# Kernel optimization log

Hardware: AMD Instinct MI355X
Metric: run time of the kernel (lower is better)

The kernel has to match this reference:

```python
import jax, jax.numpy as jnp
import numpy as np

N, E, G, F_IN, D = 50000, 400000, 256, 79, 400
BN_EPS = 1e-5


def setup_inputs() -> dict:
    key = jax.random.key(0)
    ks = jax.random.split(key, 16)
    w = lambda k, s: jax.random.normal(k, s, dtype=jnp.float32) * 0.05
    return {
        "x": jax.random.normal(ks[0], (N, F_IN), dtype=jnp.float32),
        "edge_index": jax.random.randint(ks[1], (2, E), 0, N, dtype=jnp.int32),
        "batch_index": jnp.sort(jax.random.randint(ks[2], (N,), 0, G, dtype=jnp.int32)),
        "num_graphs": G,
        "mlp1_w1": w(ks[3], (F_IN, D)), "mlp1_b1": jnp.zeros(D, jnp.float32),
        "mlp1_bn_g": jnp.ones(D, jnp.float32), "mlp1_bn_b": jnp.zeros(D, jnp.float32),
        "mlp1_bn_m": jnp.zeros(D, jnp.float32), "mlp1_bn_v": jnp.ones(D, jnp.float32),
        "mlp1_w2": w(ks[4], (D, D)), "mlp1_b2": jnp.zeros(D, jnp.float32),
        "mlp2_w1": w(ks[5], (D, D)), "mlp2_b1": jnp.zeros(D, jnp.float32),
        "mlp2_bn_g": jnp.ones(D, jnp.float32), "mlp2_bn_b": jnp.zeros(D, jnp.float32),
        "mlp2_bn_m": jnp.zeros(D, jnp.float32), "mlp2_bn_v": jnp.ones(D, jnp.float32),
        "mlp2_w2": w(ks[6], (D, D)), "mlp2_b2": jnp.zeros(D, jnp.float32),
        "out1_w": w(ks[7], (D, D)), "out1_b": jnp.zeros(D, jnp.float32),
        "out2_w": w(ks[8], (D, D)), "out2_b": jnp.zeros(D, jnp.float32),
        "out3_w": w(ks[9], (D, D)), "out3_b": jnp.zeros(D, jnp.float32),
        "out_w": w(ks[10], (2 * D, 1)), "out_b": jnp.zeros(1, jnp.float32),
        "eps1": jnp.full((1,), 5e-5, jnp.float32),
        "eps2": jnp.full((1,), 5e-5, jnp.float32),
        "eps3": jnp.full((1,), 5e-5, jnp.float32),
    }


def _bn(z, g, b, m, v):
    # BatchNorm1d in inference mode (running stats)
    return (z - m) * jax.lax.rsqrt(v + BN_EPS) * g + b


def _gin(h, src, dst, eps, w1, b1, g, bb, m, v, w2, b2):
    n = h.shape[0]
    agg = jax.ops.segment_sum(h[src], dst, num_segments=n)  # [N, d] scatter-add
    z = (1.0 + eps) * h + agg
    z = jax.nn.relu(_bn(z @ w1 + b1, g, bb, m, v))
    return jax.nn.relu(z @ w2 + b2)


def reference(x, edge_index, batch_index, num_graphs,
              mlp1_w1, mlp1_b1, mlp1_bn_g, mlp1_bn_b, mlp1_bn_m, mlp1_bn_v, mlp1_w2, mlp1_b2,
              mlp2_w1, mlp2_b1, mlp2_bn_g, mlp2_bn_b, mlp2_bn_m, mlp2_bn_v, mlp2_w2, mlp2_b2,
              out1_w, out1_b, out2_w, out2_b, out3_w, out3_b, out_w, out_b,
              eps1, eps2, eps3):
    src, dst = edge_index[0], edge_index[1]
    h = _gin(x, src, dst, eps1[0], mlp1_w1, mlp1_b1, mlp1_bn_g, mlp1_bn_b, mlp1_bn_m, mlp1_bn_v, mlp1_w2, mlp1_b2)
    h = jnp.tanh(h @ out1_w + out1_b)
    h = _gin(h, src, dst, eps2[0], mlp2_w1, mlp2_b1, mlp2_bn_g, mlp2_bn_b, mlp2_bn_m, mlp2_bn_v, mlp2_w2, mlp2_b2)
    h = jnp.tanh(h @ out2_w + out2_b)
    h = _gin(h, src, dst, eps3[0], mlp2_w1, mlp2_b1, mlp2_bn_g, mlp2_bn_b, mlp2_bn_m, mlp2_bn_v, mlp2_w2, mlp2_b2)
    h = jnp.tanh(h @ out3_w + out3_b)
    # dropout is identity in eval mode
    mx = jax.ops.segment_max(h, batch_index, num_segments=num_graphs)   # global_max_pool
    sm = jax.ops.segment_sum(h, batch_index, num_segments=num_graphs)
    cnt = jax.ops.segment_sum(jnp.ones((h.shape[0], 1), h.dtype), batch_index, num_segments=num_graphs)
    mn = sm / jnp.maximum(cnt, 1.0)                                      # global_mean_pool
    pooled = jnp.concatenate([mx, mn], axis=1)                           # [G, 2D]
    return pooled @ out_w + out_b
```

## Files before the change

### kernel.cpp

```cpp
#include <hip/hip_runtime.h>
#include <math.h>

#define NN 50000
#define NE 400000
#define NG 256
#define FIN 79
#define DD 400
#define LDK 448
#define LDK1 128
#define XP 80
#define NPAD 512
#define BK 64
#define MT ((NN + 127) / 128)
#define BN_EPS_F 1e-5f

#define SCAN_B 256
#define SCAN_NB ((NN + SCAN_B - 1) / SCAN_B)

typedef unsigned short u16;
typedef unsigned short ushort8 __attribute__((ext_vector_type(8)));
typedef unsigned short ushort4v __attribute__((ext_vector_type(4)));
typedef short short8 __attribute__((ext_vector_type(8)));
typedef float floatx4 __attribute__((ext_vector_type(4)));

__device__ inline u16 f2bf(float f) {
    unsigned int u = __builtin_bit_cast(unsigned int, f);
    u += 0x7fffu + ((u >> 16) & 1u);
    return (u16)(u >> 16);
}
__device__ inline float bf2f(u16 s) {
    unsigned int u = ((unsigned int)s) << 16;
    return __builtin_bit_cast(float, u);
}
__device__ inline float fast_tanh(float x) {
    float e = __expf(2.0f * x);
    return 1.0f - 2.0f / (e + 1.0f);
}

__device__ __forceinline__ void gld_lds16(const u16* g, u16* l) {
    __builtin_amdgcn_global_load_lds(
        (const __attribute__((address_space(1))) unsigned int*)(size_t)(g),
        (__attribute__((address_space(3))) unsigned int*)(unsigned int)(size_t)(l),
        16, 0, 0);
}

__global__ void k_gstart(const int* __restrict__ batch, int* __restrict__ gstart) {
    int g = blockIdx.x * blockDim.x + threadIdx.x;
    if (g > NG) return;
    int lo = 0, hi = NN;
    while (lo < hi) {
        int mid = (lo + hi) >> 1;
        if (batch[mid] < g) lo = mid + 1; else hi = mid;
    }
    gstart[g] = lo;
}

__global__ void k_zero_int(int* __restrict__ p, int n) {
    int i = blockIdx.x * blockDim.x + threadIdx.x;
    if (i < n) p[i] = 0;
}
__global__ void k_hist(const int* __restrict__ dst, int* __restrict__ deg) {
    int e = blockIdx.x * blockDim.x + threadIdx.x;
    if (e < NE) atomicAdd(&deg[dst[e]], 1);
}

__global__ void k_scan_a(const int* __restrict__ deg, int* __restrict__ bsum) {
    __shared__ int red[SCAN_B];
    int i = blockIdx.x * SCAN_B + threadIdx.x;
    red[threadIdx.x] = (i < NN) ? deg[i] : 0;
    __syncthreads();
    for (int s = SCAN_B / 2; s > 0; s >>= 1) {
        if (threadIdx.x < s) red[threadIdx.x] += red[threadIdx.x + s];
        __syncthreads();
    }
    if (threadIdx.x == 0) bsum[blockIdx.x] = red[0];
}
__global__ void k_scan_b(const int* __restrict__ bsum, int* __restrict__ boff) {
    __shared__ int buf[SCAN_B];
    int t = threadIdx.x;
    int v = (t < SCAN_NB) ? bsum[t] : 0;
    buf[t] = v;
    __syncthreads();
    for (int off = 1; off < SCAN_B; off <<= 1) {
        int add = (t >= off) ? buf[t - off] : 0;
        __syncthreads();
        buf[t] += add;
        __syncthreads();
    }
    if (t < SCAN_NB) boff[t] = buf[t] - v;
}
__global__ void k_scan_c(const int* __restrict__ deg, const int* __restrict__ boff,
                         int* __restrict__ rowptr, int* __restrict__ cursor) {
    __shared__ int buf[SCAN_B];
    int b = blockIdx.x;
    int i = b * SCAN_B + threadIdx.x;
    int v = (i < NN) ? deg[i] : 0;
    buf[threadIdx.x] = v;
    __syncthreads();
    for (int off = 1; off < SCAN_B; off <<= 1) {
        int add = (threadIdx.x >= off) ? buf[threadIdx.x - off] : 0;
        __syncthreads();
        buf[threadIdx.x] += add;
        __syncthreads();
    }
    int excl = boff[b] + buf[threadIdx.x] - v;
    if (i < NN) { rowptr[i] = excl; cursor[i] = excl; }
    if (b == 0 && threadIdx.x == 0) rowptr[NN] = NE;
}

__global__ void k_fill(const int* __restrict__ src, const int* __restrict__ dst,
                       int* __restrict__ cursor, int* __restrict__ eidx) {
    int e = blockIdx.x * blockDim.x + threadIdx.x;
    if (e < NE) {
        int pos = atomicAdd(&cursor[dst[e]], 1);
        eidx[pos] = src[e];
    }
}

__global__ void k_packw(const float* __restrict__ W, int K, u16* __restrict__ Wt, int ldk) {
    int idx = blockIdx.x * 256 + threadIdx.x;
    int total = NPAD * ldk;
    if (idx >= total) return;
    int n = idx / ldk, k = idx - n * ldk;
    float v = (n < DD && k < K) ? W[(size_t)k * DD + n] : 0.0f;
    Wt[idx] = f2bf(v);
}

__global__ __launch_bounds__(256)
void k_packx(const float* __restrict__ x, u16* __restrict__ xb) {
    int idx = blockIdx.x * 256 + threadIdx.x;
    if (idx >= NN * XP) return;
    int n = idx / XP, c = idx - n * XP;
    xb[idx] = (c < FIN) ? f2bf(x[(size_t)n * FIN + c]) : (u16)0;
}

__global__ __launch_bounds__(256)
void k_agg1(const u16* __restrict__ xb, const int* __restrict__ rowptr,
            const int* __restrict__ eidx, const float* __restrict__ eps,
            u16* __restrict__ z0) {
    int wave = threadIdx.x >> 6, lane = threadIdx.x & 63;
    int n = blockIdx.x * 4 + wave;
    if (lane >= 32) return;
    u16* zr = z0 + (size_t)n * LDK1;
    if (lane >= 20) {
        ushort4v zz = {0, 0, 0, 0};
        *(ushort4v*)&zr[XP + (lane - 20) * 4] = zz;
        return;
    }
    float s = 1.0f + eps[0];
    int c4 = lane * 4;
    ushort4v v = *(const ushort4v*)&xb[(size_t)n * XP + c4];
    float a[4];
    #pragma unroll
    for (int t = 0; t < 4; ++t) a[t] = s * bf2f(v[t]);
    int e0 = rowptr[n], e1 = rowptr[n + 1];
    int i = e0;
    for (; i + 2 <= e1; i += 2) {
        int s0 = eidx[i], s1 = eidx[i + 1];
        ushort4v v0 = *(const ushort4v*)&xb[(size_t)s0 * XP + c4];
        ushort4v v1 = *(const ushort4v*)&xb[(size_t)s1 * XP + c4];
        #pragma unroll
        for (int t = 0; t < 4; ++t) a[t] += bf2f(v0[t]) + bf2f(v1[t]);
    }
    if (i < e1) {
        int s0 = eidx[i];
        ushort4v v0 = *(const ushort4v*)&xb[(size_t)s0 * XP + c4];
        #pragma unroll
        for (int t = 0; t < 4; ++t) a[t] += bf2f(v0[t]);
    }
    ushort4v o;
    #pragma unroll
    for (int t = 0; t < 4; ++t) o[t] = f2bf(a[t]);
    *(ushort4v*)&zr[c4] = o;
}

__global__ __launch_bounds__(256)
void k_agg(const u16* __restrict__ h, const int* __restrict__ rowptr,
           const int* __restrict__ eidx, const float* __restrict__ eps,
           u16* __restrict__ z) {
    int wave = threadIdx.x >> 6, lane = threadIdx.x & 63;
    int n = blockIdx.x * 4 + wave;
    if (lane >= 56) return;
    float s = 1.0f + eps[0];
    int c8 = lane * 8;
    ushort8 v = *(const ushort8*)(h + (size_t)n * LDK + c8);
    float a[8];
    #pragma unroll
    for (int t = 0; t < 8; ++t) a[t] = s * bf2f(v[t]);
    int e0 = rowptr[n], e1 = rowptr[n + 1];
    int i = e0;
    for (; i + 2 <= e1; i += 2) {
        int s0 = eidx[i], s1 = eidx[i + 1];
        ushort8 v0 = *(const ushort8*)(h + (size_t)s0 * LDK + c8);
        ushort8 v1 = *(const ushort8*)(h + (size_t)s1 * LDK + c8);
        #pragma unroll
        for (int t = 0; t < 8; ++t) a[t] += bf2f(v0[t]) + bf2f(v1[t]);
    }
    if (i < e1) {
        int s0 = eidx[i];
        ushort8 v0 = *(const ushort8*)(h + (size_t)s0 * LDK + c8);
        #pragma unroll
        for (int t = 0; t < 8; ++t) a[t] += bf2f(v0[t]);
    }
    ushort8 o;
    #pragma unroll
    for (int t = 0; t < 8; ++t) o[t] = f2bf(a[t]);
    *(ushort8*)(z + (size_t)n * LDK + c8) = o;
}

#define CSTR 136
__global__ __launch_bounds__(256, 4)
void k_gemm(const u16* __restrict__ A, int lda, int ktiles,
            const u16* __restrict__ Wt,
            const float* __restrict__ bias,
            const float* __restrict__ bng, const float* __restrict__ bnb,
            const float* __restrict__ bnm, const float* __restrict__ bnv,
            u16* __restrict__ Y, int mode)
{
    __shared__ u16 smem[128 * CSTR];
    u16* As = smem;
    u16* Bs = smem + 128 * BK;
    u16* Cs = smem;

    int id = blockIdx.x;
    int mt = (id >> 5) * 8 + (id & 7);
    int nt = (id & 31) >> 3;
    if (mt >= MT) return;
    int m0 = mt * 128;
    int n0 = nt * 128;

    int tid = threadIdx.x;
    int wave = tid >> 6, lane = tid & 63;
    int wm = wave & 1, wn = wave >> 1;

    int srow = lane >> 3;
    int sc   = lane & 7;
    int lm = lane & 15;
    int q  = lane >> 4;

    bool nactive = (n0 + wn * 64) < LDK;

    floatx4 acc[4][4] = {};

    for (int kt = 0; kt < ktiles; ++kt) {
        int k0 = kt * BK;
        #pragma unroll
        for (int j = 0; j < 4; ++j) {
            int row = wave * 32 + j * 8 + srow;
            int cs = sc ^ (row & 7);
            int gr = m0 + row; gr = gr < NN ? gr : NN - 1;
            gld_lds16(A + (size_t)gr * lda + k0 + (cs << 3),
                      &As[(wave * 32 + j * 8) * BK]);
            gld_lds16(Wt + (size_t)(n0 + row) * lda + k0 + (cs << 3),
                      &Bs[(wave * 32 + j * 8) * BK]);
        }
        __syncthreads();

        if (nactive) {
            #pragma unroll
            for (int ks = 0; ks < 2; ++ks) {
                short8 af[4], bf[4];
                #pragma unroll
                for (int i = 0; i < 4; ++i) {
                    int r = wm * 64 + i * 16 + lm;
                    int ch = (ks * 4 + q) ^ (r & 7);
                    af[i] = *(const short8*)&As[r * BK + ch * 8];
                }
                #pragma unroll
                for (int j = 0; j < 4; ++j) {
                    int r = wn * 64 + j * 16 + lm;
                    int ch = (ks * 4 + q) ^ (r & 7);
                    bf[j] = *(const short8*)&Bs[r * BK + ch * 8];
                }
                #pragma unroll
                for (int i = 0; i < 4; ++i)
                    #pragma unroll
                    for (int j = 0; j < 4; ++j)
                        acc[i][j] = __builtin_amdgcn_mfma_f32_16x16x32_bf16(af[i], bf[j], acc[i][j], 0, 0, 0);
            }
        }
        __syncthreads();
    }

    #pragma unroll
    for (int j = 0; j < 4; ++j) {
        int nl = wn * 64 + j * 16 + lm;
        int n  = n0 + nl;
        bool live = n < DD;
        float bias_c = 0.0f, sc2 = 1.0f, sh = 0.0f;
        if (live) {
            bias_c = bias[n];
            if (mode == 0) {
                sc2 = bng[n] * rsqrtf(bnv[n] + BN_EPS_F);
                sh = bnb[n] - bnm[n] * sc2;
            }
        }
        #pragma unroll
        for (int i = 0; i < 4; ++i) {
            int rl = wm * 64 + i * 16 + q * 4;
            #pragma unroll
            for (int r = 0; r < 4; ++r) {
                u16 o = 0;
                if (live) {
                    float val = acc[i][j][r] + bias_c;
                    if (mode == 0)      val = fmaxf(fmaf(val, sc2, sh), 0.0f);
                    else if (mode == 1) val = fmaxf(val, 0.0f);
                    else                val = fast_tanh(val);
                    o = f2bf(val);
                }
                Cs[(rl + r) * CSTR + nl] = o;
            }
        }
    }
    __syncthreads();

    int row = tid >> 1, half = tid & 1;
    int m = m0 + row;
    if (m < NN) {
        #pragma unroll
        for (int k = 0; k < 8; ++k) {
            int coloff = half * 64 + k * 8;
            int n = n0 + coloff;
            if (n < LDK) {
                ushort8 v = *(const ushort8*)&Cs[row * CSTR + coloff];
                *(ushort8*)&Y[(size_t)m * LDK + n] = v;
            }
        }
    }
}

__global__ void k_pool(const u16* __restrict__ t3, const int* __restrict__ gstart,
                       float* __restrict__ pooled) {
    int g = blockIdx.x;
    int c = blockIdx.y * 128 + threadIdx.x;
    if (c >= DD) return;
    int s = gstart[g], e = gstart[g + 1];
    float mx = -INFINITY, sm = 0.0f;
    for (int n = s; n < e; ++n) {
        float v = bf2f(t3[(size_t)n * LDK + c]);
        mx = fmaxf(mx, v);
        sm += v;
    }
    float cnt = (float)(e - s);
    pooled[(size_t)g * 2 * DD + c] = mx;
    pooled[(size_t)g * 2 * DD + DD + c] = sm / fmaxf(cnt, 1.0f);
}

__global__ void k_final(const float* __restrict__ pooled, const float* __restrict__ w,
                        const float* __restrict__ b, float* __restrict__ out) {
    __shared__ float red[256];
    int g = blockIdx.x;
    float p = 0.0f;
    for (int j = threadIdx.x; j < 2 * DD; j += blockDim.x)
        p += pooled[(size_t)g * 2 * DD + j] * w[j];
    red[threadIdx.x] = p;
    __syncthreads();
    for (int s = 128; s > 0; s >>= 1) {
        if (threadIdx.x < s) red[threadIdx.x] += red[threadIdx.x + s];
        __syncthreads();
    }
    if (threadIdx.x == 0) out[g] = red[0] + b[0];
}

extern "C" void kernel_launch(void* const* d_in, const int* in_sizes, int n_in,
                              void* d_out, int out_size, void* d_ws, size_t ws_size,
                              hipStream_t stream) {
    const float* x     = (const float*)d_in[0];
    const int*   ei    = (const int*)d_in[1];
    const int*   batch = (const int*)d_in[2];
    const float* m1w1  = (const float*)d_in[4];
    const float* m1b1  = (const float*)d_in[5];
    const float* m1g   = (const float*)d_in[6];
    const float* m1bb  = (const float*)d_in[7];
    const float* m1m   = (const float*)d_in[8];
    const float* m1v   = (const float*)d_in[9];
    const float* m1w2  = (const float*)d_in[10];
    const float* m1b2  = (const float*)d_in[11];
    const float* m2w1  = (const float*)d_in[12];
    const float* m2b1  = (const float*)d_in[13];
    const float* m2g   = (const float*)d_in[14];
    const float* m2bb  = (const float*)d_in[15];
    const float* m2m   = (const float*)d_in[16];
    const float* m2v   = (const float*)d_in[17];
    const float* m2w2  = (const float*)d_in[18];
    const float* m2b2  = (const float*)d_in[19];
    const float* o1w   = (const float*)d_in[20];
    const float* o1b   = (const float*)d_in[21];
    const float* o2w   = (const float*)d_in[22];
    const float* o2b   = (const float*)d_in[23];
    const float* o3w   = (const float*)d_in[24];
    const float* o3b   = (const float*)d_in[25];
    const float* ow    = (const float*)d_in[26];
    const float* ob    = (const float*)d_in[27];
    const float* eps1  = (const float*)d_in[28];
    const float* eps2  = (const float*)d_in[29];
    const float* eps3  = (const float*)d_in[30];
    const int* srcI = ei;
    const int* dstI = ei + NE;

    u16* buf1 = (u16*)d_ws;
    u16* buf2 = buf1 + (size_t)NN * LDK;
    u16* buf3 = buf2 + (size_t)NN * LDK;
    u16* z0   = buf3 + (size_t)NN * LDK;
    u16* w1t  = z0 + (size_t)NN * LDK1;
    u16* m1w2t = w1t + (size_t)NPAD * LDK1;
    u16* m2w1t = m1w2t + (size_t)NPAD * LDK;
    u16* m2w2t = m2w1t + (size_t)NPAD * LDK;
    u16* o1t   = m2w2t + (size_t)NPAD * LDK;
    u16* o2t   = o1t + (size_t)NPAD * LDK;
    u16* o3t   = o2t + (size_t)NPAD * LDK;
    u16* xb    = o3t + (size_t)NPAD * LDK;
    float* pooled = (float*)(xb + (size_t)NN * XP);
    int* gstart = (int*)(pooled + (size_t)NG * 2 * DD);
    int* rowptr = gstart + (NG + 2);
    int* cursor = rowptr + (NN + 1);
    int* deg    = cursor + NN;
    int* eidx   = deg + NN;
    int* bsum   = eidx + NE;
    int* boff   = bsum + SCAN_NB;

    float* out = (float*)d_out;

    int gemmBlocks = ((MT + 7) / 8) * 32;

    k_gstart<<<2, 256, 0, stream>>>(batch, gstart);
    k_zero_int<<<(NN + 255) / 256, 256, 0, stream>>>(deg, NN);
    k_hist<<<(NE + 255) / 256, 256, 0, stream>>>(dstI, deg);
    k_scan_a<<<SCAN_NB, SCAN_B, 0, stream>>>(deg, bsum);
    k_scan_b<<<1, SCAN_B, 0, stream>>>(bsum, boff);
    k_scan_c<<<SCAN_NB, SCAN_B, 0, stream>>>(deg, boff, rowptr, cursor);
    k_fill<<<(NE + 255) / 256, 256, 0, stream>>>(srcI, dstI, cursor, eidx);

    int pw1 = (NPAD * LDK1 + 255) / 256;
    int pw = (NPAD * LDK + 255) / 256;
    k_packw<<<pw1, 256, 0, stream>>>(m1w1, FIN, w1t, LDK1);
    k_packw<<<pw, 256, 0, stream>>>(m1w2, DD, m1w2t, LDK);
    k_packw<<<pw, 256, 0, stream>>>(m2w1, DD, m2w1t, LDK);
    k_packw<<<pw, 256, 0, stream>>>(m2w2, DD, m2w2t, LDK);
    k_packw<<<pw, 256, 0, stream>>>(o1w, DD, o1t, LDK);
    k_packw<<<pw, 256, 0, stream>>>(o2w, DD, o2t, LDK);
    k_packw<<<pw, 256, 0, stream>>>(o3w, DD, o3t, LDK);
    k_packx<<<(NN * XP + 255) / 256, 256, 0, stream>>>(x, xb);

    k_agg1<<<NN / 4, 256, 0, stream>>>(xb, rowptr, eidx, eps1, z0);
    k_gemm<<<gemmBlocks, 256, 0, stream>>>(z0, LDK1, LDK1 / BK, w1t, m1b1,
                                           m1g, m1bb, m1m, m1v, buf1, 0);
    k_gemm<<<gemmBlocks, 256, 0, stream>>>(buf1, LDK, LDK / BK, m1w2t, m1b2,
                                           nullptr, nullptr, nullptr, nullptr, buf2, 1);
    k_gemm<<<gemmBlocks, 256, 0, stream>>>(buf2, LDK, LDK / BK, o1t, o1b,
                                           nullptr, nullptr, nullptr, nullptr, buf3, 2);

    k_agg<<<NN / 4, 256, 0, stream>>>(buf3, rowptr, eidx, eps2, buf1);
    k_gemm<<<gemmBlocks, 256, 0, stream>>>(buf1, LDK, LDK / BK, m2w1t, m2b1,
                                           m2g, m2bb, m2m, m2v, buf2, 0);
    k_gemm<<<gemmBlocks, 256, 0, stream>>>(buf2, LDK, LDK / BK, m2w2t, m2b2,
                                           nullptr, nullptr, nullptr, nullptr, buf1, 1);
    k_gemm<<<gemmBlocks, 256, 0, stream>>>(buf1, LDK, LDK / BK, o2t, o2b,
                                           nullptr, nullptr, nullptr, nullptr, buf2, 2);

    k_agg<<<NN / 4, 256, 0, stream>>>(buf2, rowptr, eidx, eps3, buf1);
    k_gemm<<<gemmBlocks, 256, 0, stream>>>(buf1, LDK, LDK / BK, m2w1t, m2b1,
                                           m2g, m2bb, m2m, m2v, buf3, 0);
    k_gemm<<<gemmBlocks, 256, 0, stream>>>(buf3, LDK, LDK / BK, m2w2t, m2b2,
                                           nullptr, nullptr, nullptr, nullptr, buf1, 1);
    k_gemm<<<gemmBlocks, 256, 0, stream>>>(buf1, LDK, LDK / BK, o3t, o3b,
                                           nullptr, nullptr, nullptr, nullptr, buf3, 2);

    k_pool<<<dim3(NG, 4), 128, 0, stream>>>(buf3, gstart, pooled);
    k_final<<<NG, 256, 0, stream>>>(pooled, ow, ob, out);
}
```

Measured before the change: 868.3 us.

## Prefetch GEMM tiles through registers, vectorize pooling, trim padded aggregation lanes

The GEMM no longer uses direct global-to-LDS loads. It keeps the next K-tile in registers while the current tile is computed, so global load latency overlaps with the MFMA work, and it relaxes the launch-bounds occupancy hint from 4 to 3. Global pooling now uses one 256-thread block per graph: four waves stride over the nodes with 8-wide vector loads and are combined through LDS, replacing scalar per-column loops. Aggregation skips the padded columns 400-447, which cuts wasted gathers but leaves those padding columns of z unwritten, so correctness depends on them already holding zeros from earlier writes.

```diff
diff --git a/kernel.cpp b/kernel.cpp
--- a/kernel.cpp
+++ b/kernel.cpp
@@ -37,13 +37,6 @@
     return 1.0f - 2.0f / (e + 1.0f);
 }
 
-__device__ __forceinline__ void gld_lds16(const u16* g, u16* l) {
-    __builtin_amdgcn_global_load_lds(
-        (const __attribute__((address_space(1))) unsigned int*)(size_t)(g),
-        (__attribute__((address_space(3))) unsigned int*)(unsigned int)(size_t)(l),
-        16, 0, 0);
-}
-
 __global__ void k_gstart(const int* __restrict__ batch, int* __restrict__ gstart) {
     int g = blockIdx.x * blockDim.x + threadIdx.x;
     if (g > NG) return;
@@ -180,7 +173,7 @@
            u16* __restrict__ z) {
     int wave = threadIdx.x >> 6, lane = threadIdx.x & 63;
     int n = blockIdx.x * 4 + wave;
-    if (lane >= 56) return;
+    if (lane >= 50) return;
     float s = 1.0f + eps[0];
     int c8 = lane * 8;
     ushort8 v = *(const ushort8*)(h + (size_t)n * LDK + c8);
@@ -209,7 +202,7 @@
 }
 
 #define CSTR 136
-__global__ __launch_bounds__(256, 4)
+__global__ __launch_bounds__(256, 3)
 void k_gemm(const u16* __restrict__ A, int lda, int ktiles,
             const u16* __restrict__ Wt,
             const float* __restrict__ bias,
@@ -235,27 +228,45 @@
 
     int srow = lane >> 3;
     int sc   = lane & 7;
+    int swz  = (sc ^ srow) << 3;
     int lm = lane & 15;
     int q  = lane >> 4;
 
     bool nactive = (n0 + wn * 64) < LDK;
 
+    const u16* gA[4]; const u16* gB[4];
+    int lofs[4];
+    #pragma unroll
+    for (int j = 0; j < 4; ++j) {
+        int rowL = wave * 32 + j * 8 + srow;
+        lofs[j] = rowL * BK + swz;
+        int gr = m0 + rowL; gr = gr < NN ? gr : NN - 1;
+        gA[j] = A + (size_t)gr * lda + sc * 8;
+        gB[j] = Wt + (size_t)(n0 + rowL) * lda + sc * 8;
+    }
+
+    ushort8 va[4], vb[4];
+    #pragma unroll
+    for (int j = 0; j < 4; ++j) { va[j] = *(const ushort8*)gA[j]; vb[j] = *(const ushort8*)gB[j]; }
+
     floatx4 acc[4][4] = {};
 
     for (int kt = 0; kt < ktiles; ++kt) {
-        int k0 = kt * BK;
+        __syncthreads();
         #pragma unroll
         for (int j = 0; j < 4; ++j) {
-            int row = wave * 32 + j * 8 + srow;
-            int cs = sc ^ (row & 7);
-            int gr = m0 + row; gr = gr < NN ? gr : NN - 1;
-            gld_lds16(A + (size_t)gr * lda + k0 + (cs << 3),
-                      &As[(wave * 32 + j * 8) * BK]);
-            gld_lds16(Wt + (size_t)(n0 + row) * lda + k0 + (cs << 3),
-                      &Bs[(wave * 32 + j * 8) * BK]);
-        }
-        __syncthreads();
-
+            *(ushort8*)&As[lofs[j]] = va[j];
+            *(ushort8*)&Bs[lofs[j]] = vb[j];
+        }
+        __syncthreads();
+        if (kt + 1 < ktiles) {
+            int ko = (kt + 1) * BK;
+            #pragma unroll
+            for (int j = 0; j < 4; ++j) {
+                va[j] = *(const ushort8*)(gA[j] + ko);
+                vb[j] = *(const ushort8*)(gB[j] + ko);
+            }
+        }
         if (nactive) {
             #pragma unroll
             for (int ks = 0; ks < 2; ++ks) {
@@ -263,13 +274,13 @@
                 #pragma unroll
                 for (int i = 0; i < 4; ++i) {
                     int r = wm * 64 + i * 16 + lm;
-                    int ch = (ks * 4 + q) ^ (r & 7);
+                    int ch = (ks * 4 + q) ^ (lm & 7);
                     af[i] = *(const short8*)&As[r * BK + ch * 8];
                 }
                 #pragma unroll
                 for (int j = 0; j < 4; ++j) {
                     int r = wn * 64 + j * 16 + lm;
-                    int ch = (ks * 4 + q) ^ (r & 7);
+                    int ch = (ks * 4 + q) ^ (lm & 7);
                     bf[j] = *(const short8*)&Bs[r * BK + ch * 8];
                 }
                 #pragma unroll
@@ -279,8 +290,8 @@
                         acc[i][j] = __builtin_amdgcn_mfma_f32_16x16x32_bf16(af[i], bf[j], acc[i][j], 0, 0, 0);
             }
         }
-        __syncthreads();
-    }
+    }
+    __syncthreads();
 
     #pragma unroll
     for (int j = 0; j < 4; ++j) {
@@ -308,7 +319,7 @@
                     else                val = fast_tanh(val);
                     o = f2bf(val);
                 }
-                Cs[(rl + r) * CSTR + nl] = o;
+                if (nactive) Cs[(rl + r) * CSTR + nl] = o;
             }
         }
     }
@@ -329,21 +340,42 @@
     }
 }
 
-__global__ void k_pool(const u16* __restrict__ t3, const int* __restrict__ gstart,
-                       float* __restrict__ pooled) {
+__global__ __launch_bounds__(256)
+void k_pool(const u16* __restrict__ t3, const int* __restrict__ gstart,
+            float* __restrict__ pooled) {
+    __shared__ float smax[4][408];
+    __shared__ float ssum[4][408];
     int g = blockIdx.x;
-    int c = blockIdx.y * 128 + threadIdx.x;
-    if (c >= DD) return;
+    int wave = threadIdx.x >> 6, lane = threadIdx.x & 63;
     int s = gstart[g], e = gstart[g + 1];
-    float mx = -INFINITY, sm = 0.0f;
-    for (int n = s; n < e; ++n) {
-        float v = bf2f(t3[(size_t)n * LDK + c]);
-        mx = fmaxf(mx, v);
-        sm += v;
-    }
-    float cnt = (float)(e - s);
-    pooled[(size_t)g * 2 * DD + c] = mx;
-    pooled[(size_t)g * 2 * DD + DD + c] = sm / fmaxf(cnt, 1.0f);
+    if (lane < 50) {
+        int c8 = lane * 8;
+        float mx[8], sm[8];
+        #pragma unroll
+        for (int t = 0; t < 8; ++t) { mx[t] = -INFINITY; sm[t] = 0.0f; }
+        for (int n = s + wave; n < e; n += 4) {
+            ushort8 v = *(const ushort8*)&t3[(size_t)n * LDK + c8];
+            #pragma unroll
+            for (int t = 0; t < 8; ++t) {
+                float f = bf2f(v[t]);
+                mx[t] = fmaxf(mx[t], f);
+                sm[t] += f;
+            }
+        }
+        #pragma unroll
+        for (int t = 0; t < 8; ++t) {
+            smax[wave][c8 + t] = mx[t];
+            ssum[wave][c8 + t] = sm[t];
+        }
+    }
+    __syncthreads();
+    float cnt = fmaxf((float)(e - s), 1.0f);
+    for (int c = threadIdx.x; c < DD; c += 256) {
+        float m = fmaxf(fmaxf(smax[0][c], smax[1][c]), fmaxf(smax[2][c], smax[3][c]));
+        float su = ssum[0][c] + ssum[1][c] + ssum[2][c] + ssum[3][c];
+        pooled[(size_t)g * 2 * DD + c] = m;
+        pooled[(size_t)g * 2 * DD + DD + c] = su / cnt;
+    }
 }
 
 __global__ void k_final(const float* __restrict__ pooled, const float* __restrict__ w,
@@ -466,6 +498,6 @@
     k_gemm<<<gemmBlocks, 256, 0, stream>>>(buf1, LDK, LDK / BK, o3t, o3b,
                                            nullptr, nullptr, nullptr, nullptr, buf3, 2);
 
-    k_pool<<<dim3(NG, 4), 128, 0, stream>>>(buf3, gstart, pooled);
+    k_pool<<<NG, 256, 0, stream>>>(buf3, gstart, pooled);
     k_final<<<NG, 256, 0, stream>>>(pooled, ow, ob, out);
 }
```

Result: no change. 876.1 us (+0.9%).
